# Performance work log

Hardware: AMD Instinct MI355X
Metric: run time of the kernel (lower is better)

## Reference

```python
import jax, jax.numpy as jnp
import numpy as np

B, D0, D1 = 4096, 128, 128
T, DEPTH, W = 64, 2, 4          # num_tree, depth, width
S = W ** (DEPTH + 1)            # num_state = 64
NODES = sum(W ** l for l in range(DEPTH + 1))  # 21 internal nodes per tree
D = D0 + D1


def setup_inputs() -> dict:
    key = jax.random.key(0)
    ks = jax.random.split(key, 9)
    inp0 = jax.random.normal(ks[0], (B, D0), jnp.float32)
    inp1 = jax.random.normal(ks[1], (B, D1), jnp.float32)
    x2 = jax.random.normal(ks[2], (B,), jnp.float32)
    # ForestLinear: per-tree, per-node linear maps to `width` branch logits
    W_nodes = 0.02 * jax.random.normal(ks[3], (T, NODES, D, W), jnp.float32)
    b_nodes = jnp.zeros((T, NODES, W), jnp.float32)
    # MultiDense([0,1], 1): per-(tree,state) linear probe per input
    W0 = 0.02 * jax.random.normal(ks[4], (T, S, D0), jnp.float32)
    b0 = jnp.zeros((T, S), jnp.float32)
    W1 = 0.02 * jax.random.normal(ks[5], (T, S, D1), jnp.float32)
    b1 = jnp.zeros((T, S), jnp.float32)
    return {"inp0": inp0, "inp1": inp1, "x2": x2,
            "W_nodes": W_nodes, "b_nodes": b_nodes,
            "W0": W0, "b0": b0, "W1": W1, "b1": b1}


def _forest_states(x, W_nodes, b_nodes):
    # x: [B, D] -> leaf-state probabilities [B, T, S]
    logits = jnp.einsum('bd,tndw->btnw', x, W_nodes) + b_nodes  # [B,T,NODES,W]
    probs = jax.nn.softmax(logits, axis=-1)
    p = jnp.ones((x.shape[0], T, 1), probs.dtype)
    off = 0
    for l in range(DEPTH + 1):
        n = W ** l
        pl = probs[:, :, off:off + n, :]                 # [B,T,n,W]
        p = (p[..., None] * pl).reshape(x.shape[0], T, n * W)
        off += n
    return p  # [B, T, S]


def reference(inp0, inp1, x2, W_nodes, b_nodes, W0, b0, W1, b1):
    x_states = _forest_states(jnp.concatenate([inp0, inp1], axis=-1), W_nodes, b_nodes)
    # per-tree/state linear probes; equivalent to tile + MultiDense, no materialized tile
    x_pred = (jnp.einsum('bd,tsd->bts', inp0, W0) + b0
              + jnp.einsum('bd,tsd->bts', inp1, W1) + b1)  # [B,T,S]
    y_pred_logit_parallel = x2[:, None, None] + x_pred
    ave_pred_tree = jnp.sum(x_states * jax.nn.sigmoid(y_pred_logit_parallel), axis=2)  # [B,T]
    ave_pred = jnp.mean(ave_pred_tree, axis=1)  # [B]
    return (y_pred_logit_parallel, ave_pred)
```

## Files before the change

### kernel.cpp

```cpp
#include <hip/hip_runtime.h>

#define B_SZ    4096
#define DD      256
#define T_TREES 64
#define NNODES  21
#define S_LEAF  64
#define M_TILE  128
#define QBYTES  20480
#define WBYTES  (4 * QBYTES)
#define XOFF    ((size_t)T_TREES * WBYTES)


typedef __attribute__((ext_vector_type(8))) short  short8;
typedef __attribute__((ext_vector_type(4))) float  f32x4;

__device__ __forceinline__ unsigned short f2bf(float f) {
    unsigned int u = __float_as_uint(f);
    u += 0x7fffu + ((u >> 16) & 1u);
    return (unsigned short)(u >> 16);
}
__device__ __forceinline__ void gl2lds16(const void* g, void* l) {
    __builtin_amdgcn_global_load_lds(
        (const __attribute__((address_space(1))) unsigned int*)g,
        (__attribute__((address_space(3))) unsigned int*)l, 16, 0, 0);
}
__device__ __host__ __forceinline__ int woffq(int c, int klo) {
    return (c >> 1) * 256 + (((((klo << 1) ^ (c & 14))) | (c & 1)) << 4);
}

__global__ void zero_ave_kernel(float* __restrict__ out1) {
    int i = blockIdx.x * 256 + threadIdx.x;
    if (i < B_SZ) out1[i] = 0.0f;
}

__global__ void prep_weights(const float* __restrict__ Wn, const float* __restrict__ W0,
                             const float* __restrict__ W1, const float* __restrict__ inp0,
                             const float* __restrict__ inp1, char* __restrict__ ws,
                             float* __restrict__ out1) {
    int id = blockIdx.x * 256 + threadIdx.x;
    if (id < 43008) {
        int oct  = id & 31;
        int rest = id >> 5;
        int n    = rest % NNODES;
        int t    = rest / NNODES;
        int q    = oct >> 3, klo = oct & 7;
        const f32x4* src = (const f32x4*)(Wn + (((size_t)t * NNODES + n) * DD + oct * 8) * 4);
        f32x4 v[8];
        #pragma unroll
        for (int j = 0; j < 8; ++j) v[j] = src[j];
        char* base = ws + (size_t)t * WBYTES + q * QBYTES;
        #pragma unroll
        for (int w = 0; w < 4; ++w) {
            int c = n * 4 + w + (n >= 5 ? 12 : 0);
            short8 pack;
            #pragma unroll
            for (int j = 0; j < 8; ++j) pack[j] = (short)f2bf(v[j][w]);
            *(short8*)(base + woffq(c, klo)) = pack;
        }
    } else if (id < 67584) {
        int idx  = id - 43008;
        int kc   = idx & 31;
        int rest = idx >> 5;
        int c    = 20 + rest % 12;
        int t    = rest / 12;
        short8 z = (short8){0,0,0,0,0,0,0,0};
        *(short8*)(ws + (size_t)t * WBYTES + (kc >> 3) * QBYTES + woffq(c, kc & 7)) = z;
    } else if (id < 198656) {
        int idx = id - 67584;
        int kc  = idx & 31;
        int s   = (idx >> 5) & 63;
        int t   = idx >> 11;
        int k0  = kc * 8;
        const float* src = (k0 < 128) ? (W0 + ((size_t)t * S_LEAF + s) * 128 + k0)
                                      : (W1 + ((size_t)t * S_LEAF + s) * 128 + (k0 - 128));
        short8 pack;
        #pragma unroll
        for (int j = 0; j < 8; ++j) pack[j] = (short)f2bf(src[j]);
        *(short8*)(ws + (size_t)t * WBYTES + (kc >> 3) * QBYTES + woffq(96 + s, kc & 7)) = pack;
    } else if (id < 202752) {
        out1[id - 198656] = 0.0f;
    } else if (id < 333824) {
        int idx = id - 202752;
        int oct = idx & 31;
        int r   = idx >> 5;
        const float* src = (oct < 16) ? (inp0 + (size_t)r * 128 + oct * 8)
                                      : (inp1 + (size_t)r * 128 + (oct - 16) * 8);
        f32x4 f0 = *(const f32x4*)src;
        f32x4 f1 = *(const f32x4*)(src + 4);
        short8 pack;
        pack[0]=(short)f2bf(f0[0]); pack[1]=(short)f2bf(f0[1]);
        pack[2]=(short)f2bf(f0[2]); pack[3]=(short)f2bf(f0[3]);
        pack[4]=(short)f2bf(f1[0]); pack[5]=(short)f2bf(f1[1]);
        pack[6]=(short)f2bf(f1[2]); pack[7]=(short)f2bf(f1[3]);
        *(short8*)(ws + XOFF + ((size_t)r * DD + oct * 8) * 2) = pack;
    }
}

__global__ __launch_bounds__(256, 3)
void forest_main(const float* __restrict__ x2,  const float* __restrict__ bn,
                 const float* __restrict__ b0,  const float* __restrict__ b1,
                 const char* __restrict__ wsW,
                 float* __restrict__ out0, float* __restrict__ out1) {
    __shared__ __align__(16) char smem[2 * QBYTES];

    const int tid  = threadIdx.x;
    const int orig = blockIdx.x;
    const int swz  = (orig & 7) * 256 + (orig >> 3);
    const int t    = swz >> 5;
    const int mt   = swz & 31;
    const int m0   = mt * M_TILE;
    const int lane = tid & 63;
    const int wid  = tid >> 6;
    const int ri   = lane & 15;
    const int kg   = lane >> 4;

    const unsigned short* xbf = (const unsigned short*)(wsW + XOFF);
    const char* wbase = wsW + (size_t)t * WBYTES;

    f32x4 acc[2][10];
    #pragma unroll
    for (int sr = 0; sr < 2; ++sr)
        #pragma unroll
        for (int ct = 0; ct < 10; ++ct)
            acc[sr][ct] = (f32x4){0.f, 0.f, 0.f, 0.f};

    const int gr0r = m0 + wid * 32 + ri;
    const int gr1r = gr0r + 16;

    int dsb[2];
    #pragma unroll
    for (int kkl = 0; kkl < 2; ++kkl) {
        int klo = kkl * 4 + kg;
        dsb[kkl] = (ri >> 1) * 256 + (((((klo << 1) ^ (ri & 14))) | (ri & 1)) << 4);
    }

    {
        const char* src = wbase + tid * 16;
        char* dst = smem + tid * 16;
        #pragma unroll
        for (int it = 0; it < 5; ++it)
            gl2lds16(src + it * 4096, dst + it * 4096);
    }
    short8 a00 = *(const short8*)(xbf + (size_t)gr0r * DD + 0 * 32 + kg * 8);
    short8 a10 = *(const short8*)(xbf + (size_t)gr1r * DD + 0 * 32 + kg * 8);
    short8 a01 = *(const short8*)(xbf + (size_t)gr0r * DD + 1 * 32 + kg * 8);
    short8 a11 = *(const short8*)(xbf + (size_t)gr1r * DD + 1 * 32 + kg * 8);

    #pragma unroll
    for (int q = 0; q < 4; ++q) {
        __syncthreads();
        short8 n00, n10, n01, n11;
        if (q < 3) {
            const char* src = wbase + (q + 1) * QBYTES + tid * 16;
            char* dst = smem + ((q + 1) & 1) * QBYTES + tid * 16;
            #pragma unroll
            for (int it = 0; it < 5; ++it)
                gl2lds16(src + it * 4096, dst + it * 4096);
            n00 = *(const short8*)(xbf + (size_t)gr0r * DD + (2*q+2) * 32 + kg * 8);
            n10 = *(const short8*)(xbf + (size_t)gr1r * DD + (2*q+2) * 32 + kg * 8);
            n01 = *(const short8*)(xbf + (size_t)gr0r * DD + (2*q+3) * 32 + kg * 8);
            n11 = *(const short8*)(xbf + (size_t)gr1r * DD + (2*q+3) * 32 + kg * 8);
        }
        const char* bufp = smem + (q & 1) * QBYTES;
        #pragma unroll
        for (int ct = 0; ct < 10; ++ct) {
            short8 b0f = *(const short8*)(bufp + dsb[0] + ct * 2048);
            acc[0][ct] = __builtin_amdgcn_mfma_f32_16x16x32_bf16(a00, b0f, acc[0][ct], 0, 0, 0);
            acc[1][ct] = __builtin_amdgcn_mfma_f32_16x16x32_bf16(a10, b0f, acc[1][ct], 0, 0, 0);
        }
        #pragma unroll
        for (int ct = 0; ct < 10; ++ct) {
            short8 b1f = *(const short8*)(bufp + dsb[1] + ct * 2048);
            acc[0][ct] = __builtin_amdgcn_mfma_f32_16x16x32_bf16(a01, b1f, acc[0][ct], 0, 0, 0);
            acc[1][ct] = __builtin_amdgcn_mfma_f32_16x16x32_bf16(a11, b1f, acc[1][ct], 0, 0, 0);
        }
        a00 = n00; a10 = n10; a01 = n01; a11 = n11;
    }

    const int kgbase = kg * 16;
    #pragma unroll
    for (int sr = 0; sr < 2; ++sr) {
        const int rlBase = wid * 32 + sr * 16 + kg * 4;
        const int gr0 = m0 + rlBase;
        f32x4 x2v = *(const f32x4*)(x2 + gr0);
        float bn0 = bn[t * 84 + ri];
        float bn1 = bn[t * 84 + 16 + (ri & 3)];

        float L1r[4];
        #pragma unroll
        for (int r = 0; r < 4; ++r) {
            float v0 = acc[sr][0][r] + bn0;
            float e0 = __expf(v0);
            float s0 = e0 + __shfl_xor(e0, 1); s0 += __shfl_xor(s0, 2);
            float p0 = e0 * __builtin_amdgcn_rcpf(s0);
            float v1 = acc[sr][1][r] + bn1;
            float e1 = __expf(v1);
            float s1 = e1 + __shfl_xor(e1, 1); s1 += __shfl_xor(s1, 2);
            float p1 = e1 * __builtin_amdgcn_rcpf(s1);
            float pa  = __shfl(p0, kgbase + (ri >> 2));
            float pb0 = __shfl(p0, kgbase + ((ri + 4) & 15));
            float pb1 = __shfl(p1, kgbase + ((ri + 4) & 15));
            L1r[r] = pa * ((ri < 12) ? pb0 : pb1);
        }
        float partial[4] = {0.f, 0.f, 0.f, 0.f};
        #pragma unroll
        for (int ct = 0; ct < 4; ++ct) {
            int s = ct * 16 + ri;
            float bn2 = bn[t * 84 + 20 + s];
            float bb  = b0[t * S_LEAF + s] + b1[t * S_LEAF + s];
            #pragma unroll
            for (int r = 0; r < 4; ++r) {
                float v = acc[sr][2 + ct][r] + bn2;
                float e = __expf(v);
                float ss = e + __shfl_xor(e, 1); ss += __shfl_xor(ss, 2);
                float p2 = e * __builtin_amdgcn_rcpf(ss);
                float L2 = p2 * __shfl(L1r[r], kgbase + ct * 4 + (ri >> 2));
                float y = acc[sr][6 + ct][r] + x2v[r] + bb;
                out0[((size_t)(gr0 + r) * T_TREES + t) * S_LEAF + s] = y;
                float sg = __builtin_amdgcn_rcpf(1.0f + __expf(-y));
                partial[r] += sg * L2;
            }
        }
        #pragma unroll
        for (int r = 0; r < 4; ++r) {
            float p = partial[r];
            p += __shfl_xor(p, 1); p += __shfl_xor(p, 2);
            p += __shfl_xor(p, 4); p += __shfl_xor(p, 8);
            if (ri == 0) atomicAdd(out1 + gr0 + r, p * (1.0f / T_TREES));
        }
    }
}

__device__ __forceinline__ short8 ldAraw(const float* __restrict__ inp0,
                                         const float* __restrict__ inp1,
                                         int gr, int kkidx, int kg) {
    int k0 = kkidx * 32 + kg * 8;
    const float* src = (k0 < 128) ? (inp0 + (size_t)gr * 128 + k0)
                                  : (inp1 + (size_t)gr * 128 + (k0 - 128));
    f32x4 f0 = *(const f32x4*)src;
    f32x4 f1 = *(const f32x4*)(src + 4);
    short8 a;
    a[0]=(short)f2bf(f0[0]); a[1]=(short)f2bf(f0[1]);
    a[2]=(short)f2bf(f0[2]); a[3]=(short)f2bf(f0[3]);
    a[4]=(short)f2bf(f1[0]); a[5]=(short)f2bf(f1[1]);
    a[6]=(short)f2bf(f1[2]); a[7]=(short)f2bf(f1[3]);
    return a;
}

__global__ __launch_bounds__(256, 2)
void forest_fb(const float* __restrict__ inp0, const float* __restrict__ inp1,
               const float* __restrict__ x2,   const float* __restrict__ Wn,
               const float* __restrict__ bn,   const float* __restrict__ W0,
               const float* __restrict__ b0,   const float* __restrict__ W1,
               const float* __restrict__ b1,
               float* __restrict__ out0, float* __restrict__ out1) {
    __shared__ __align__(16) char smem[QBYTES];

    const int tid  = threadIdx.x;
    const int orig = blockIdx.x;
    const int swz  = (orig & 7) * 256 + (orig >> 3);
    const int t    = swz >> 5;
    const int mt   = swz & 31;
    const int m0   = mt * 128;
    const int lane = tid & 63;
    const int wid  = tid >> 6;
    const int ri   = lane & 15;
    const int kg   = lane >> 4;

    f32x4 acc[2][10];
    #pragma unroll
    for (int sr = 0; sr < 2; ++sr)
        #pragma unroll
        for (int ct = 0; ct < 10; ++ct)
            acc[sr][ct] = (f32x4){0.f, 0.f, 0.f, 0.f};

    const int gr0r = m0 + wid * 32 + ri;
    const int gr1r = gr0r + 16;

    int dsb[2];
    #pragma unroll
    for (int kkl = 0; kkl < 2; ++kkl) {
        int klo = kkl * 4 + kg;
        dsb[kkl] = (ri >> 1) * 256 + (((((klo << 1) ^ (ri & 14))) | (ri & 1)) << 4);
    }

    for (int q = 0; q < 4; ++q) {
        #pragma unroll
        for (int it = 0; it < 5; ++it) {
            int idx = tid + it * 256;
            int c   = idx >> 3;
            int klo = idx & 7;
            int k0  = (q * 8 + klo) * 8;
            unsigned short v[8];
            if (c < 20) {
                int n = c >> 2, w = c & 3;
                const float* src = Wn + (((size_t)t * NNODES + n) * DD + k0) * 4 + w;
                #pragma unroll
                for (int j = 0; j < 8; ++j) v[j] = f2bf(src[j * 4]);
            } else if (c < 32) {
                #pragma unroll
                for (int j = 0; j < 8; ++j) v[j] = 0;
            } else if (c < 96) {
                int n = 5 + ((c - 32) >> 2), w = (c - 32) & 3;
                const float* src = Wn + (((size_t)t * NNODES + n) * DD + k0) * 4 + w;
                #pragma unroll
                for (int j = 0; j < 8; ++j) v[j] = f2bf(src[j * 4]);
            } else {
                int s = c - 96;
                const float* src = (k0 < 128) ? (W0 + ((size_t)t * S_LEAF + s) * 128 + k0)
                                              : (W1 + ((size_t)t * S_LEAF + s) * 128 + (k0 - 128));
                #pragma unroll
                for (int j = 0; j < 8; ++j) v[j] = f2bf(src[j]);
            }
            short8 pack;
            #pragma unroll
            for (int j = 0; j < 8; ++j) pack[j] = (short)v[j];
            *(short8*)(smem + woffq(c, klo)) = pack;
        }
        short8 a00 = ldAraw(inp0, inp1, gr0r, 2*q+0, kg);
        short8 a10 = ldAraw(inp0, inp1, gr1r, 2*q+0, kg);
        short8 a01 = ldAraw(inp0, inp1, gr0r, 2*q+1, kg);
        short8 a11 = ldAraw(inp0, inp1, gr1r, 2*q+1, kg);
        __syncthreads();
        #pragma unroll
        for (int ct = 0; ct < 10; ++ct) {
            short8 b0f = *(const short8*)(smem + dsb[0] + ct * 2048);
            acc[0][ct] = __builtin_amdgcn_mfma_f32_16x16x32_bf16(a00, b0f, acc[0][ct], 0, 0, 0);
            acc[1][ct] = __builtin_amdgcn_mfma_f32_16x16x32_bf16(a10, b0f, acc[1][ct], 0, 0, 0);
        }
        #pragma unroll
        for (int ct = 0; ct < 10; ++ct) {
            short8 b1f = *(const short8*)(smem + dsb[1] + ct * 2048);
            acc[0][ct] = __builtin_amdgcn_mfma_f32_16x16x32_bf16(a01, b1f, acc[0][ct], 0, 0, 0);
            acc[1][ct] = __builtin_amdgcn_mfma_f32_16x16x32_bf16(a11, b1f, acc[1][ct], 0, 0, 0);
        }
        if (q < 3) __syncthreads();
    }

    const int kgbase = kg * 16;
    #pragma unroll
    for (int sr = 0; sr < 2; ++sr) {
        const int rlBase = wid * 32 + sr * 16 + kg * 4;
        const int gr0 = m0 + rlBase;
        f32x4 x2v = *(const f32x4*)(x2 + gr0);
        float bn0 = bn[t * 84 + ri];
        float bn1 = bn[t * 84 + 16 + (ri & 3)];
        float L1r[4];
        #pragma unroll
        for (int r = 0; r < 4; ++r) {
            float v0 = acc[sr][0][r] + bn0;
            float e0 = __expf(v0);
            float s0 = e0 + __shfl_xor(e0, 1); s0 += __shfl_xor(s0, 2);
            float p0 = e0 * __builtin_amdgcn_rcpf(s0);
            float v1 = acc[sr][1][r] + bn1;
            float e1 = __expf(v1);
            float s1 = e1 + __shfl_xor(e1, 1); s1 += __shfl_xor(s1, 2);
            float p1 = e1 * __builtin_amdgcn_rcpf(s1);
            float pa  = __shfl(p0, kgbase + (ri >> 2));
            float pb0 = __shfl(p0, kgbase + ((ri + 4) & 15));
            float pb1 = __shfl(p1, kgbase + ((ri + 4) & 15));
            L1r[r] = pa * ((ri < 12) ? pb0 : pb1);
        }
        float partial[4] = {0.f, 0.f, 0.f, 0.f};
        #pragma unroll
        for (int ct = 0; ct < 4; ++ct) {
            int s = ct * 16 + ri;
            float bn2 = bn[t * 84 + 20 + s];
            float bb  = b0[t * S_LEAF + s] + b1[t * S_LEAF + s];
            #pragma unroll
            for (int r = 0; r < 4; ++r) {
                float v = acc[sr][2 + ct][r] + bn2;
                float e = __expf(v);
                float ss = e + __shfl_xor(e, 1); ss += __shfl_xor(ss, 2);
                float p2 = e * __builtin_amdgcn_rcpf(ss);
                float L2 = p2 * __shfl(L1r[r], kgbase + ct * 4 + (ri >> 2));
                float y = acc[sr][6 + ct][r] + x2v[r] + bb;
                out0[((size_t)(gr0 + r) * T_TREES + t) * S_LEAF + s] = y;
                float sg = __builtin_amdgcn_rcpf(1.0f + __expf(-y));
                partial[r] += sg * L2;
            }
        }
        #pragma unroll
        for (int r = 0; r < 4; ++r) {
            float p = partial[r];
            p += __shfl_xor(p, 1); p += __shfl_xor(p, 2);
            p += __shfl_xor(p, 4); p += __shfl_xor(p, 8);
            if (ri == 0) atomicAdd(out1 + gr0 + r, p * (1.0f / T_TREES));
        }
    }
}

extern "C" void kernel_launch(void* const* d_in, const int* in_sizes, int n_in,
                              void* d_out, int out_size, void* d_ws, size_t ws_size,
                              hipStream_t stream) {
    const float* inp0 = (const float*)d_in[0];
    const float* inp1 = (const float*)d_in[1];
    const float* x2   = (const float*)d_in[2];
    const float* Wn   = (const float*)d_in[3];
    const float* bn   = (const float*)d_in[4];
    const float* W0   = (const float*)d_in[5];
    const float* b0   = (const float*)d_in[6];
    const float* W1   = (const float*)d_in[7];
    const float* b1   = (const float*)d_in[8];

    float* out0 = (float*)d_out;
    float* out1 = out0 + (size_t)B_SZ * T_TREES * S_LEAF;

    const size_t need = XOFF + (size_t)B_SZ * DD * 2;
    dim3 grid((B_SZ / M_TILE) * T_TREES);

    if (ws_size >= need) {
        hipLaunchKernelGGL(prep_weights, dim3(1304), dim3(256), 0, stream,
                           Wn, W0, W1, inp0, inp1, (char*)d_ws, out1);
        hipLaunchKernelGGL(forest_main, grid, dim3(256), 0, stream,
                           x2, bn, b0, b1, (const char*)d_ws, out0, out1);
    } else {
        hipLaunchKernelGGL(zero_ave_kernel, dim3((B_SZ + 255) / 256), dim3(256), 0, stream, out1);
        hipLaunchKernelGGL(forest_fb, grid, dim3(256), 0, stream,
                           inp0, inp1, x2, Wn, bn, W0, b0, W1, b1, out0, out1);
    }
}
```

Baseline: 59.77 us.

## Stage weights in two half-K chunks and use DPP for softmax reductions

Replaces the four-quarter double-buffered weight staging with two 40KB half-K loads into a single LDS buffer, using a new per-column swizzle layout. A-fragments are now loaded inside the K loop rather than prefetched, and load/compute overlap within a block is dropped. The epilogue replaces ds-based shuffle reductions and the rotate shuffle with DPP row operations (quad_perm and row_ror/shr) to cut LDS traffic. The change keeps the same LDS footprint but removes intra-block prefetch, so it relies on other resident blocks to hide load latency.

```diff
diff --git a/kernel.cpp b/kernel.cpp
--- a/kernel.cpp
+++ b/kernel.cpp
@@ -6,13 +6,29 @@
 #define NNODES  21
 #define S_LEAF  64
 #define M_TILE  128
+#define HBYTES  40960
+#define WBYTES  (2 * HBYTES)
+#define XOFF    ((size_t)T_TREES * WBYTES)
 #define QBYTES  20480
-#define WBYTES  (4 * QBYTES)
-#define XOFF    ((size_t)T_TREES * WBYTES)
 
 
 typedef __attribute__((ext_vector_type(8))) short  short8;
 typedef __attribute__((ext_vector_type(4))) float  f32x4;
+
+#define DPP_ADD(x, ctrl) ((x) + __int_as_float(__builtin_amdgcn_mov_dpp(__float_as_int(x), (ctrl), 0xF, 0xF, true)))
+#define DPP_MOV(x, ctrl) __int_as_float(__builtin_amdgcn_mov_dpp(__float_as_int(x), (ctrl), 0xF, 0xF, true))
+__device__ __forceinline__ float qsum4(float x) {
+    x = DPP_ADD(x, 0xB1);
+    x = DPP_ADD(x, 0x4E);
+    return x;
+}
+__device__ __forceinline__ float rsum16(float x) {
+    x = DPP_ADD(x, 0xB1);
+    x = DPP_ADD(x, 0x4E);
+    x = DPP_ADD(x, 0x124);
+    x = DPP_ADD(x, 0x128);
+    return x;
+}
 
 __device__ __forceinline__ unsigned short f2bf(float f) {
     unsigned int u = __float_as_uint(f);
@@ -23,6 +39,9 @@
     __builtin_amdgcn_global_load_lds(
         (const __attribute__((address_space(1))) unsigned int*)g,
         (__attribute__((address_space(3))) unsigned int*)l, 16, 0, 0);
+}
+__device__ __host__ __forceinline__ int woffh(int c, int klo) {
+    return c * 256 + (((klo ^ c) & 15) << 4);
 }
 __device__ __host__ __forceinline__ int woffq(int c, int klo) {
     return (c >> 1) * 256 + (((((klo << 1) ^ (c & 14))) | (c & 1)) << 4);
@@ -43,19 +62,19 @@
         int rest = id >> 5;
         int n    = rest % NNODES;
         int t    = rest / NNODES;
-        int q    = oct >> 3, klo = oct & 7;
+        int h    = oct >> 4, klo = oct & 15;
         const f32x4* src = (const f32x4*)(Wn + (((size_t)t * NNODES + n) * DD + oct * 8) * 4);
         f32x4 v[8];
         #pragma unroll
         for (int j = 0; j < 8; ++j) v[j] = src[j];
-        char* base = ws + (size_t)t * WBYTES + q * QBYTES;
+        char* base = ws + (size_t)t * WBYTES + h * HBYTES;
         #pragma unroll
         for (int w = 0; w < 4; ++w) {
             int c = n * 4 + w + (n >= 5 ? 12 : 0);
             short8 pack;
             #pragma unroll
             for (int j = 0; j < 8; ++j) pack[j] = (short)f2bf(v[j][w]);
-            *(short8*)(base + woffq(c, klo)) = pack;
+            *(short8*)(base + woffh(c, klo)) = pack;
         }
     } else if (id < 67584) {
         int idx  = id - 43008;
@@ -64,7 +83,7 @@
         int c    = 20 + rest % 12;
         int t    = rest / 12;
         short8 z = (short8){0,0,0,0,0,0,0,0};
-        *(short8*)(ws + (size_t)t * WBYTES + (kc >> 3) * QBYTES + woffq(c, kc & 7)) = z;
+        *(short8*)(ws + (size_t)t * WBYTES + (kc >> 4) * HBYTES + woffh(c, kc & 15)) = z;
     } else if (id < 198656) {
         int idx = id - 67584;
         int kc  = idx & 31;
@@ -76,7 +95,7 @@
         short8 pack;
         #pragma unroll
         for (int j = 0; j < 8; ++j) pack[j] = (short)f2bf(src[j]);
-        *(short8*)(ws + (size_t)t * WBYTES + (kc >> 3) * QBYTES + woffq(96 + s, kc & 7)) = pack;
+        *(short8*)(ws + (size_t)t * WBYTES + (kc >> 4) * HBYTES + woffh(96 + s, kc & 15)) = pack;
     } else if (id < 202752) {
         out1[id - 198656] = 0.0f;
     } else if (id < 333824) {
@@ -101,7 +120,7 @@
                  const float* __restrict__ b0,  const float* __restrict__ b1,
                  const char* __restrict__ wsW,
                  float* __restrict__ out0, float* __restrict__ out1) {
-    __shared__ __align__(16) char smem[2 * QBYTES];
+    __shared__ __align__(16) char smem[HBYTES];
 
     const int tid  = threadIdx.x;
     const int orig = blockIdx.x;
@@ -127,54 +146,31 @@
     const int gr0r = m0 + wid * 32 + ri;
     const int gr1r = gr0r + 16;
 
-    int dsb[2];
-    #pragma unroll
-    for (int kkl = 0; kkl < 2; ++kkl) {
-        int klo = kkl * 4 + kg;
-        dsb[kkl] = (ri >> 1) * 256 + (((((klo << 1) ^ (ri & 14))) | (ri & 1)) << 4);
-    }
-
-    {
-        const char* src = wbase + tid * 16;
-        char* dst = smem + tid * 16;
-        #pragma unroll
-        for (int it = 0; it < 5; ++it)
-            gl2lds16(src + it * 4096, dst + it * 4096);
-    }
-    short8 a00 = *(const short8*)(xbf + (size_t)gr0r * DD + 0 * 32 + kg * 8);
-    short8 a10 = *(const short8*)(xbf + (size_t)gr1r * DD + 0 * 32 + kg * 8);
-    short8 a01 = *(const short8*)(xbf + (size_t)gr0r * DD + 1 * 32 + kg * 8);
-    short8 a11 = *(const short8*)(xbf + (size_t)gr1r * DD + 1 * 32 + kg * 8);
-
-    #pragma unroll
-    for (int q = 0; q < 4; ++q) {
+    for (int h = 0; h < 2; ++h) {
+        {
+            const char* src = wbase + h * HBYTES + tid * 16;
+            char* dst = smem + tid * 16;
+            #pragma unroll
+            for (int it = 0; it < 10; ++it)
+                gl2lds16(src + it * 4096, dst + it * 4096);
+        }
         __syncthreads();
-        short8 n00, n10, n01, n11;
-        if (q < 3) {
-            const char* src = wbase + (q + 1) * QBYTES + tid * 16;
-            char* dst = smem + ((q + 1) & 1) * QBYTES + tid * 16;
-            #pragma unroll
-            for (int it = 0; it < 5; ++it)
-                gl2lds16(src + it * 4096, dst + it * 4096);
-            n00 = *(const short8*)(xbf + (size_t)gr0r * DD + (2*q+2) * 32 + kg * 8);
-            n10 = *(const short8*)(xbf + (size_t)gr1r * DD + (2*q+2) * 32 + kg * 8);
-            n01 = *(const short8*)(xbf + (size_t)gr0r * DD + (2*q+3) * 32 + kg * 8);
-            n11 = *(const short8*)(xbf + (size_t)gr1r * DD + (2*q+3) * 32 + kg * 8);
-        }
-        const char* bufp = smem + (q & 1) * QBYTES;
-        #pragma unroll
-        for (int ct = 0; ct < 10; ++ct) {
-            short8 b0f = *(const short8*)(bufp + dsb[0] + ct * 2048);
-            acc[0][ct] = __builtin_amdgcn_mfma_f32_16x16x32_bf16(a00, b0f, acc[0][ct], 0, 0, 0);
-            acc[1][ct] = __builtin_amdgcn_mfma_f32_16x16x32_bf16(a10, b0f, acc[1][ct], 0, 0, 0);
-        }
-        #pragma unroll
-        for (int ct = 0; ct < 10; ++ct) {
-            short8 b1f = *(const short8*)(bufp + dsb[1] + ct * 2048);
-            acc[0][ct] = __builtin_amdgcn_mfma_f32_16x16x32_bf16(a01, b1f, acc[0][ct], 0, 0, 0);
-            acc[1][ct] = __builtin_amdgcn_mfma_f32_16x16x32_bf16(a11, b1f, acc[1][ct], 0, 0, 0);
-        }
-        a00 = n00; a10 = n10; a01 = n01; a11 = n11;
+
+        #pragma unroll
+        for (int ks = 0; ks < 4; ++ks) {
+            const int kk = h * 4 + ks;
+            short8 a0 = *(const short8*)(xbf + (size_t)gr0r * DD + kk * 32 + kg * 8);
+            short8 a1 = *(const short8*)(xbf + (size_t)gr1r * DD + kk * 32 + kg * 8);
+            const int klo = ks * 4 + kg;
+            const int dsB = ri * 256 + (((klo ^ ri) & 15) << 4);
+            #pragma unroll
+            for (int ct = 0; ct < 10; ++ct) {
+                short8 bv = *(const short8*)(smem + dsB + ct * 4096);
+                acc[0][ct] = __builtin_amdgcn_mfma_f32_16x16x32_bf16(a0, bv, acc[0][ct], 0, 0, 0);
+                acc[1][ct] = __builtin_amdgcn_mfma_f32_16x16x32_bf16(a1, bv, acc[1][ct], 0, 0, 0);
+            }
+        }
+        if (h == 0) __syncthreads();
     }
 
     const int kgbase = kg * 16;
@@ -189,17 +185,13 @@
         float L1r[4];
         #pragma unroll
         for (int r = 0; r < 4; ++r) {
-            float v0 = acc[sr][0][r] + bn0;
-            float e0 = __expf(v0);
-            float s0 = e0 + __shfl_xor(e0, 1); s0 += __shfl_xor(s0, 2);
-            float p0 = e0 * __builtin_amdgcn_rcpf(s0);
-            float v1 = acc[sr][1][r] + bn1;
-            float e1 = __expf(v1);
-            float s1 = e1 + __shfl_xor(e1, 1); s1 += __shfl_xor(s1, 2);
-            float p1 = e1 * __builtin_amdgcn_rcpf(s1);
+            float e0 = __expf(acc[sr][0][r] + bn0);
+            float p0 = e0 * __builtin_amdgcn_rcpf(qsum4(e0));
+            float e1 = __expf(acc[sr][1][r] + bn1);
+            float p1 = e1 * __builtin_amdgcn_rcpf(qsum4(e1));
             float pa  = __shfl(p0, kgbase + (ri >> 2));
-            float pb0 = __shfl(p0, kgbase + ((ri + 4) & 15));
-            float pb1 = __shfl(p1, kgbase + ((ri + 4) & 15));
+            float pb0 = DPP_MOV(p0, 0x124);
+            float pb1 = DPP_MOV(p1, 0x124);
             L1r[r] = pa * ((ri < 12) ? pb0 : pb1);
         }
         float partial[4] = {0.f, 0.f, 0.f, 0.f};
@@ -210,10 +202,8 @@
             float bb  = b0[t * S_LEAF + s] + b1[t * S_LEAF + s];
             #pragma unroll
             for (int r = 0; r < 4; ++r) {
-                float v = acc[sr][2 + ct][r] + bn2;
-                float e = __expf(v);
-                float ss = e + __shfl_xor(e, 1); ss += __shfl_xor(ss, 2);
-                float p2 = e * __builtin_amdgcn_rcpf(ss);
+                float e = __expf(acc[sr][2 + ct][r] + bn2);
+                float p2 = e * __builtin_amdgcn_rcpf(qsum4(e));
                 float L2 = p2 * __shfl(L1r[r], kgbase + ct * 4 + (ri >> 2));
                 float y = acc[sr][6 + ct][r] + x2v[r] + bb;
                 out0[((size_t)(gr0 + r) * T_TREES + t) * S_LEAF + s] = y;
@@ -223,9 +213,7 @@
         }
         #pragma unroll
         for (int r = 0; r < 4; ++r) {
-            float p = partial[r];
-            p += __shfl_xor(p, 1); p += __shfl_xor(p, 2);
-            p += __shfl_xor(p, 4); p += __shfl_xor(p, 8);
+            float p = rsum16(partial[r]);
             if (ri == 0) atomicAdd(out1 + gr0 + r, p * (1.0f / T_TREES));
         }
     }
@@ -348,17 +336,13 @@
         float L1r[4];
         #pragma unroll
         for (int r = 0; r < 4; ++r) {
-            float v0 = acc[sr][0][r] + bn0;
-            float e0 = __expf(v0);
-            float s0 = e0 + __shfl_xor(e0, 1); s0 += __shfl_xor(s0, 2);
-            float p0 = e0 * __builtin_amdgcn_rcpf(s0);
-            float v1 = acc[sr][1][r] + bn1;
-            float e1 = __expf(v1);
-            float s1 = e1 + __shfl_xor(e1, 1); s1 += __shfl_xor(s1, 2);
-            float p1 = e1 * __builtin_amdgcn_rcpf(s1);
+            float e0 = __expf(acc[sr][0][r] + bn0);
+            float p0 = e0 * __builtin_amdgcn_rcpf(qsum4(e0));
+            float e1 = __expf(acc[sr][1][r] + bn1);
+            float p1 = e1 * __builtin_amdgcn_rcpf(qsum4(e1));
             float pa  = __shfl(p0, kgbase + (ri >> 2));
-            float pb0 = __shfl(p0, kgbase + ((ri + 4) & 15));
-            float pb1 = __shfl(p1, kgbase + ((ri + 4) & 15));
+            float pb0 = DPP_MOV(p0, 0x124);
+            float pb1 = DPP_MOV(p1, 0x124);
             L1r[r] = pa * ((ri < 12) ? pb0 : pb1);
         }
         float partial[4] = {0.f, 0.f, 0.f, 0.f};
@@ -369,10 +353,8 @@
             float bb  = b0[t * S_LEAF + s] + b1[t * S_LEAF + s];
             #pragma unroll
             for (int r = 0; r < 4; ++r) {
-                float v = acc[sr][2 + ct][r] + bn2;
-                float e = __expf(v);
-                float ss = e + __shfl_xor(e, 1); ss += __shfl_xor(ss, 2);
-                float p2 = e * __builtin_amdgcn_rcpf(ss);
+                float e = __expf(acc[sr][2 + ct][r] + bn2);
+                float p2 = e * __builtin_amdgcn_rcpf(qsum4(e));
                 float L2 = p2 * __shfl(L1r[r], kgbase + ct * 4 + (ri >> 2));
                 float y = acc[sr][6 + ct][r] + x2v[r] + bb;
                 out0[((size_t)(gr0 + r) * T_TREES + t) * S_LEAF + s] = y;
@@ -382,9 +364,7 @@
         }
         #pragma unroll
         for (int r = 0; r < 4; ++r) {
-            float p = partial[r];
-            p += __shfl_xor(p, 1); p += __shfl_xor(p, 2);
-            p += __shfl_xor(p, 4); p += __shfl_xor(p, 8);
+            float p = rsum16(partial[r]);
             if (ri == 0) atomicAdd(out1 + gr0 + r, p * (1.0f / T_TREES));
         }
     }
```

After: 52.99 us. 1.13x faster.
